# Performance work log

Measured on AMD Instinct MI355X. Metric: run time of the kernel, lower is better.

## Reference

```python
import jax, jax.numpy as jnp
import numpy as np

D_MODEL = 1024
N_HEADS = 16
HEAD_DIM = D_MODEL // N_HEADS


def setup_inputs() -> dict:
    key = jax.random.key(0)
    ks = jax.random.split(key, 5)
    B, T = 2, 2048
    x = jax.random.normal(ks[0], (B, T, D_MODEL), dtype=jnp.float32)
    s_in = 1.0 / np.sqrt(D_MODEL)
    W_qkv = jax.random.normal(ks[1], (D_MODEL, 3 * D_MODEL), dtype=jnp.float32) * s_in
    b_qkv = jnp.zeros((3 * D_MODEL,), dtype=jnp.float32)
    W_out = jax.random.normal(ks[2], (D_MODEL, D_MODEL), dtype=jnp.float32) * s_in
    b_out = jnp.zeros((D_MODEL,), dtype=jnp.float32)
    return {"x": x, "W_qkv": W_qkv, "b_qkv": b_qkv, "W_out": W_out, "b_out": b_out}


def reference(x, W_qkv, b_qkv, W_out, b_out):
    B, T, C = x.shape
    qkv = x @ W_qkv + b_qkv  # (B, T, 3C)
    q, k, v = jnp.split(qkv, 3, axis=-1)
    # (B, H, T, Dh)
    q = q.reshape(B, T, N_HEADS, HEAD_DIM).transpose(0, 2, 1, 3)
    k = k.reshape(B, T, N_HEADS, HEAD_DIM).transpose(0, 2, 1, 3)
    v = v.reshape(B, T, N_HEADS, HEAD_DIM).transpose(0, 2, 1, 3)
    scale = 1.0 / jnp.sqrt(jnp.asarray(HEAD_DIM, dtype=x.dtype))
    scores = jnp.einsum('bhqd,bhkd->bhqk', q, k) * scale  # (B, H, T, T)
    causal = jnp.tril(jnp.ones((T, T), dtype=bool))
    scores = jnp.where(causal[None, None], scores, jnp.asarray(-jnp.inf, dtype=scores.dtype))
    attn = jax.nn.softmax(scores, axis=-1)
    out = jnp.einsum('bhqk,bhkd->bhqd', attn, v)  # (B, H, T, Dh)
    out = out.transpose(0, 2, 1, 3).reshape(B, T, C)
    return out @ W_out + b_out
```

## Files before the change

kernel.cpp:

```cpp
#include <hip/hip_runtime.h>
#include <hip/hip_bf16.h>
#include <stdint.h>

typedef __bf16 bf16;
typedef __bf16 bf16x4 __attribute__((ext_vector_type(4)));
typedef __bf16 bf16x8 __attribute__((ext_vector_type(8)));
typedef float  f32x4  __attribute__((ext_vector_type(4)));

#define D_MODEL 1024
#define N_HEADS 16
#define HEAD_DIM 64
#define SEQ 2048
#define BATCH 2
#define LOG2E 1.4426950408889634f
#define NEG_SENT -3.0e4f
#define CAP 24.0f

__device__ __forceinline__ bf16x8 ld8(const bf16* p) { return *(const bf16x8*)p; }

__device__ __forceinline__ void async16(const bf16* g, bf16* l) {
  __builtin_amdgcn_global_load_lds(
      (const __attribute__((address_space(1))) void*)g,
      (__attribute__((address_space(3))) void*)l, 16, 0, 0);
}

__global__ __launch_bounds__(256)
void prep(const float* __restrict__ x, bf16* __restrict__ x16,
          const float* __restrict__ Wqkv, bf16* __restrict__ Wqkv_t,
          const float* __restrict__ Wout, bf16* __restrict__ Wout_t) {
  __shared__ float tile[32][33];
  const int blk = blockIdx.x, tid = threadIdx.x;
  if (blk < 4096) {
    int i = (blk * 256 + tid) * 4;
    float4 v = *(const float4*)&x[i];
    bf16 o[4] = {(bf16)v.x, (bf16)v.y, (bf16)v.z, (bf16)v.w};
    *(uint2*)&x16[i] = *(uint2*)o;
    return;
  }
  const float* in; bf16* out; int R, C, c0, r0;
  if (blk < 7168) {
    int b = blk - 4096;
    in = Wqkv; out = Wqkv_t; R = 1024; C = 3072;
    c0 = (b % 96) * 32; r0 = (b / 96) * 32;
  } else {
    int b = blk - 7168;
    in = Wout; out = Wout_t; R = 1024; C = 1024;
    c0 = (b % 32) * 32; r0 = (b / 32) * 32;
  }
  const int tx = tid & 31, ty = tid >> 5;
  #pragma unroll
  for (int i = 0; i < 32; i += 8)
    tile[ty + i][tx] = in[(size_t)(r0 + ty + i) * C + c0 + tx];
  __syncthreads();
  #pragma unroll
  for (int i = 0; i < 32; i += 8)
    out[(size_t)(c0 + ty + i) * R + r0 + tx] = (bf16)tile[tx][ty + i];
}

__global__ __launch_bounds__(256)
void gemm_bt(const bf16* __restrict__ A, const bf16* __restrict__ Bt,
             const float* __restrict__ bias, float* __restrict__ outf,
             bf16* __restrict__ Qp, bf16* __restrict__ Kp, bf16* __restrict__ Vtp,
             int N, int mode) {
  __shared__ __align__(16) bf16 shA[128 * 32];
  __shared__ __align__(16) bf16 shB[128 * 32];
  const int tid  = threadIdx.x;
  const int bm0  = blockIdx.y * 128, bn0 = blockIdx.x * 128;
  const int wave = tid >> 6, lane = tid & 63;
  const int quad = lane >> 4, l16 = lane & 15;
  const int wm = (wave >> 1) * 64, wn = (wave & 1) * 64;

  const int c_lo  = tid;
  const int row_lo = c_lo >> 2,  col_lo = (c_lo & 3) << 3;
  const int c_hi  = tid + 256;
  const int row_hi = c_hi >> 2,  col_hi = (c_hi & 3) << 3;
  const int cb_lo = (wave * 64) * 8;
  const int cb_hi = (256 + wave * 64) * 8;

  f32x4 acc[4][4];
  #pragma unroll
  for (int i = 0; i < 4; i++)
    #pragma unroll
    for (int j = 0; j < 4; j++)
      acc[i][j] = (f32x4){0.f, 0.f, 0.f, 0.f};

  for (int k0 = 0; k0 < 1024; k0 += 32) {
    async16(&A[(size_t)(bm0 + row_lo) * 1024 + k0 + col_lo], &shA[cb_lo]);
    async16(&A[(size_t)(bm0 + row_hi) * 1024 + k0 + col_hi], &shA[cb_hi]);
    async16(&Bt[(size_t)(bn0 + row_lo) * 1024 + k0 + col_lo], &shB[cb_lo]);
    async16(&Bt[(size_t)(bn0 + row_hi) * 1024 + k0 + col_hi], &shB[cb_hi]);
    __syncthreads();
    bf16x8 af[4], bg[4];
    #pragma unroll
    for (int i = 0; i < 4; i++)
      af[i] = ld8(&shA[(wm + i * 16 + l16) * 32 + quad * 8]);
    #pragma unroll
    for (int j = 0; j < 4; j++)
      bg[j] = ld8(&shB[(wn + j * 16 + l16) * 32 + quad * 8]);
    #pragma unroll
    for (int i = 0; i < 4; i++)
      #pragma unroll
      for (int j = 0; j < 4; j++)
        acc[i][j] = __builtin_amdgcn_mfma_f32_16x16x32_bf16(af[i], bg[j], acc[i][j], 0, 0, 0);
    __syncthreads();
  }

  #pragma unroll
  for (int i = 0; i < 4; i++) {
    #pragma unroll
    for (int j = 0; j < 4; j++) {
      int gn = bn0 + wn + j * 16 + l16;
      float bv = bias[gn];
      int gm0 = bm0 + wm + i * 16 + quad * 4;
      if (mode == 1) {
        #pragma unroll
        for (int r = 0; r < 4; r++)
          outf[(size_t)(gm0 + r) * N + gn] = acc[i][j][r] + bv;
      } else {
        int which = gn >> 10, rem = gn & 1023;
        int h = rem >> 6, d = rem & 63;
        int b = gm0 >> 11, t0 = gm0 & 2047;
        int bh = b * N_HEADS + h;
        if (which == 2) {
          bf16x4 vv = {(bf16)(acc[i][j][0] + bv), (bf16)(acc[i][j][1] + bv),
                       (bf16)(acc[i][j][2] + bv), (bf16)(acc[i][j][3] + bv)};
          *(bf16x4*)&Vtp[((size_t)bh * 64 + d) * SEQ + t0] = vv;
        } else {
          bf16* dst = (which == 0) ? Qp : Kp;
          #pragma unroll
          for (int r = 0; r < 4; r++)
            dst[((size_t)bh * SEQ + t0 + r) * 64 + d] = (bf16)(acc[i][j][r] + bv);
        }
      }
    }
  }
}

__global__ __launch_bounds__(256)
void gemm_out(const bf16* __restrict__ A, const bf16* __restrict__ Bt,
              const float* __restrict__ bias, float* __restrict__ outf) {
  __shared__ __align__(16) bf16 shA[64 * 32];
  __shared__ __align__(16) bf16 shB[128 * 32];
  const int tid  = threadIdx.x;
  const int bm0  = blockIdx.y * 64, bn0 = blockIdx.x * 128;
  const int wave = tid >> 6, lane = tid & 63;
  const int quad = lane >> 4, l16 = lane & 15;
  const int wn = wave * 32;

  f32x4 acc[4][2];
  #pragma unroll
  for (int i = 0; i < 4; i++)
    #pragma unroll
    for (int j = 0; j < 2; j++)
      acc[i][j] = (f32x4){0.f, 0.f, 0.f, 0.f};

  const int srow = tid >> 2, scol = (tid & 3) << 3;
  for (int k0 = 0; k0 < 1024; k0 += 32) {
    async16(&A[(size_t)(bm0 + srow) * 1024 + k0 + scol], &shA[tid * 8]);
    async16(&Bt[(size_t)(bn0 + srow) * 1024 + k0 + scol], &shB[tid * 8]);
    async16(&Bt[(size_t)(bn0 + 64 + srow) * 1024 + k0 + scol], &shB[(256 + tid) * 8]);
    __syncthreads();
    bf16x8 af[4], bg[2];
    #pragma unroll
    for (int i = 0; i < 4; i++)
      af[i] = ld8(&shA[(i * 16 + l16) * 32 + quad * 8]);
    #pragma unroll
    for (int j = 0; j < 2; j++)
      bg[j] = ld8(&shB[(wn + j * 16 + l16) * 32 + quad * 8]);
    #pragma unroll
    for (int i = 0; i < 4; i++)
      #pragma unroll
      for (int j = 0; j < 2; j++)
        acc[i][j] = __builtin_amdgcn_mfma_f32_16x16x32_bf16(af[i], bg[j], acc[i][j], 0, 0, 0);
    __syncthreads();
  }

  #pragma unroll
  for (int i = 0; i < 4; i++) {
    #pragma unroll
    for (int j = 0; j < 2; j++) {
      int gn = bn0 + wn + j * 16 + l16;
      float bv = bias[gn];
      int gm0 = bm0 + i * 16 + quad * 4;
      #pragma unroll
      for (int r = 0; r < 4; r++)
        outf[(size_t)(gm0 + r) * D_MODEL + gn] = acc[i][j][r] + bv;
    }
  }
}

__global__ __launch_bounds__(256)
void attn_k(const bf16* __restrict__ Qp, const bf16* __restrict__ Kp,
            const bf16* __restrict__ Vtp, bf16* __restrict__ Obuf) {
  __shared__ __align__(16) bf16 shK[2][64 * 64];
  __shared__ __align__(16) bf16 shV[2][64 * 64];
  __shared__ __align__(16) bf16 shPT[4][32 * 72];
  const int tid  = threadIdx.x;
  const int wave = tid >> 6, lane = tid & 63;
  const int quad = lane >> 4, l16 = lane & 15;
  const int bx = blockIdx.x;
  const int g = bx >> 5;
  const int qb = (g < 8) ? g : 23 - g;
  const int bh = bx & 31;
  const int qw0 = qb * 128 + wave * 32;

  const bf16* Qbh = Qp  + (size_t)bh * SEQ * 64;
  const bf16* Kbh = Kp  + (size_t)bh * SEQ * 64;
  const bf16* Vbh = Vtp + (size_t)bh * 64 * SEQ;

  const int kr_s = tid >> 3, kc_s = tid & 7;

  bf16x8 aQ[2][2];
  #pragma unroll
  for (int g2 = 0; g2 < 2; g2++)
    #pragma unroll
    for (int p = 0; p < 2; p++)
      aQ[g2][p] = ld8(&Qbh[(size_t)(qw0 + g2 * 16 + l16) * 64 + p * 32 + quad * 8]);

  f32x4 o0[4], o1[4];
  #pragma unroll
  for (int j = 0; j < 4; j++) { o0[j] = (f32x4){0.f,0.f,0.f,0.f}; o1[j] = (f32x4){0.f,0.f,0.f,0.f}; }
  f32x4 lacc0 = (f32x4){0.f,0.f,0.f,0.f}, lacc1 = (f32x4){0.f,0.f,0.f,0.f};
  const int qlane0 = qw0 + l16, qlane1 = qw0 + 16 + l16;
  const int xq = l16 & 7;

  const float SC = 0.125f * LOG2E;
  bf16* PT = shPT[wave];

  #pragma unroll
  for (int i = 0; i < 2; i++) {
    int kr = kr_s + i * 32;
    async16(&Kbh[(size_t)kr * 64 + (kc_s ^ (kr & 7)) * 8], &shK[0][(kr * 8 + kc_s) * 8]);
    async16(&Vbh[(size_t)kr * SEQ + (kc_s ^ (kr & 7)) * 8], &shV[0][(kr * 8 + kc_s) * 8]);
  }
  __syncthreads();

  const int NS = 2 * qb + 2;
  int cur = 0;
  for (int s = 0; s < NS; s++) {
    if (s + 1 < NS) {
      const int kb1 = (s + 1) * 64;
      #pragma unroll
      for (int i = 0; i < 2; i++) {
        int kr = kr_s + i * 32;
        async16(&Kbh[(size_t)(kb1 + kr) * 64 + (kc_s ^ (kr & 7)) * 8],
                &shK[cur ^ 1][(kr * 8 + kc_s) * 8]);
        async16(&Vbh[(size_t)kr * SEQ + kb1 + (kc_s ^ (kr & 7)) * 8],
                &shV[cur ^ 1][(kr * 8 + kc_s) * 8]);
      }
    }

    const int hb = s * 64;
    if (hb <= qw0 + 31) {
      const bf16* Kb = shK[cur];
      const bf16* Vb = shV[cur];

      f32x4 st0[4], st1[4];
      __builtin_amdgcn_s_setprio(1);
      #pragma unroll
      for (int c = 0; c < 4; c++) {
        int kr0 = c * 16 + l16;
        bf16x8 kf0 = ld8(&Kb[kr0 * 64 + ((quad    ) ^ xq) * 8]);
        bf16x8 kf1 = ld8(&Kb[kr0 * 64 + ((quad + 4) ^ xq) * 8]);
        f32x4 a0 = (f32x4){0.f,0.f,0.f,0.f};
        a0 = __builtin_amdgcn_mfma_f32_16x16x32_bf16(kf0, aQ[0][0], a0, 0, 0, 0);
        a0 = __builtin_amdgcn_mfma_f32_16x16x32_bf16(kf1, aQ[0][1], a0, 0, 0, 0);
        f32x4 a1 = (f32x4){0.f,0.f,0.f,0.f};
        a1 = __builtin_amdgcn_mfma_f32_16x16x32_bf16(kf0, aQ[1][0], a1, 0, 0, 0);
        a1 = __builtin_amdgcn_mfma_f32_16x16x32_bf16(kf1, aQ[1][1], a1, 0, 0, 0);
        st0[c] = a0; st1[c] = a1;
      }
      __builtin_amdgcn_s_setprio(0);

      if (hb + 63 > qw0) {
        #pragma unroll
        for (int c = 0; c < 4; c++)
          #pragma unroll
          for (int r = 0; r < 4; r++) {
            int key = hb + c * 16 + quad * 4 + r;
            if (key > qlane0) st0[c][r] = NEG_SENT;
            if (key > qlane1) st1[c][r] = NEG_SENT;
          }
      }

      #pragma unroll
      for (int c = 0; c < 4; c++) {
        #pragma unroll
        for (int r = 0; r < 4; r++) {
          st0[c][r] = exp2f(__builtin_fmaf(st0[c][r], SC, -CAP));
          st1[c][r] = exp2f(__builtin_fmaf(st1[c][r], SC, -CAP));
        }
        lacc0 += st0[c]; lacc1 += st1[c];
      }

      #pragma unroll
      for (int c = 0; c < 4; c++) {
        bf16x4 p0 = {(bf16)st0[c][0], (bf16)st0[c][1], (bf16)st0[c][2], (bf16)st0[c][3]};
        bf16x4 p1 = {(bf16)st1[c][0], (bf16)st1[c][1], (bf16)st1[c][2], (bf16)st1[c][3]};
        *(bf16x4*)&PT[l16 * 72 + c * 16 + quad * 4] = p0;
        *(bf16x4*)&PT[(16 + l16) * 72 + c * 16 + quad * 4] = p1;
      }
      asm volatile("s_waitcnt lgkmcnt(0)" ::: "memory");
      bf16x8 bP00 = ld8(&PT[l16 * 72 + quad * 8]);
      bf16x8 bP01 = ld8(&PT[l16 * 72 + 32 + quad * 8]);
      bf16x8 bP10 = ld8(&PT[(16 + l16) * 72 + quad * 8]);
      bf16x8 bP11 = ld8(&PT[(16 + l16) * 72 + 32 + quad * 8]);

      __builtin_amdgcn_s_setprio(1);
      #pragma unroll
      for (int j = 0; j < 4; j++) {
        int d = j * 16 + l16;
        bf16x8 v0 = ld8(&Vb[d * 64 + ((quad    ) ^ xq) * 8]);
        bf16x8 v1 = ld8(&Vb[d * 64 + ((quad + 4) ^ xq) * 8]);
        o0[j] = __builtin_amdgcn_mfma_f32_16x16x32_bf16(v0, bP00, o0[j], 0, 0, 0);
        o0[j] = __builtin_amdgcn_mfma_f32_16x16x32_bf16(v1, bP01, o0[j], 0, 0, 0);
        o1[j] = __builtin_amdgcn_mfma_f32_16x16x32_bf16(v0, bP10, o1[j], 0, 0, 0);
        o1[j] = __builtin_amdgcn_mfma_f32_16x16x32_bf16(v1, bP11, o1[j], 0, 0, 0);
      }
      __builtin_amdgcn_s_setprio(0);
    }

    __syncthreads();
    cur ^= 1;
  }

  const int b = bh >> 4, h = bh & 15;
  {
    float lr0 = (lacc0[0] + lacc0[1]) + (lacc0[2] + lacc0[3]);
    lr0 += __shfl_xor(lr0, 16, 64);
    lr0 += __shfl_xor(lr0, 32, 64);
    float lr1 = (lacc1[0] + lacc1[1]) + (lacc1[2] + lacc1[3]);
    lr1 += __shfl_xor(lr1, 16, 64);
    lr1 += __shfl_xor(lr1, 32, 64);
    float inv0 = 1.0f / lr0, inv1 = 1.0f / lr1;
    size_t base0 = ((size_t)(b * SEQ + qw0 + l16)) * D_MODEL + h * 64;
    size_t base1 = ((size_t)(b * SEQ + qw0 + 16 + l16)) * D_MODEL + h * 64;
    #pragma unroll
    for (int j = 0; j < 4; j++) {
      bf16x4 ov0 = {(bf16)(o0[j][0] * inv0), (bf16)(o0[j][1] * inv0),
                    (bf16)(o0[j][2] * inv0), (bf16)(o0[j][3] * inv0)};
      bf16x4 ov1 = {(bf16)(o1[j][0] * inv1), (bf16)(o1[j][1] * inv1),
                    (bf16)(o1[j][2] * inv1), (bf16)(o1[j][3] * inv1)};
      *(bf16x4*)&Obuf[base0 + j * 16 + quad * 4] = ov0;
      *(bf16x4*)&Obuf[base1 + j * 16 + quad * 4] = ov1;
    }
  }
}

extern "C" void kernel_launch(void* const* d_in, const int* in_sizes, int n_in,
                              void* d_out, int out_size, void* d_ws, size_t ws_size,
                              hipStream_t stream) {
  const float* x    = (const float*)d_in[0];
  const float* Wqkv = (const float*)d_in[1];
  const float* bqkv = (const float*)d_in[2];
  const float* Wout = (const float*)d_in[3];
  const float* bout = (const float*)d_in[4];
  float* out = (float*)d_out;

  char* ws = (char*)d_ws;
  bf16* x16    = (bf16*)(ws);
  bf16* Wqkv_t = (bf16*)(ws + 8388608);
  bf16* Wout_t = (bf16*)(ws + 14680064);
  bf16* Qp     = (bf16*)(ws + 16777216);
  bf16* Kp     = (bf16*)(ws + 25165824);
  bf16* Vtp    = (bf16*)(ws + 33554432);
  bf16* Obuf   = x16;

  prep<<<8192, 256, 0, stream>>>(x, x16, Wqkv, Wqkv_t, Wout, Wout_t);

  gemm_bt<<<dim3(3072 / 128, 4096 / 128), 256, 0, stream>>>(
      x16, Wqkv_t, bqkv, nullptr, Qp, Kp, Vtp, 3072, 0);

  attn_k<<<dim3(512), 256, 0, stream>>>(Qp, Kp, Vtp, Obuf);

  gemm_out<<<dim3(1024 / 128, 4096 / 64), 256, 0, stream>>>(
      Obuf, Wout_t, bout, out);
}
```

Baseline: 195.1 us.

## Use 512-thread attention blocks with 256-query tiles and halved P staging

The attention kernel now runs 8 waves per block, covering 256 queries instead of 128, so each K/V tile loaded into LDS is shared by twice as many waves. The grid becomes 8x32 with a simple query-block index, replacing the earlier balanced causal ordering. The per-wave P staging buffer is halved by writing the two 16-row halves one after the other, and V fragments are loaded before the P round trip. The risks are worse load balance across the causal triangle with fewer, larger blocks, fewer blocks overall (256 for 256 CUs), and extra LDS wait points.

```diff
diff --git a/kernel.cpp b/kernel.cpp
--- a/kernel.cpp
+++ b/kernel.cpp
@@ -189,20 +189,18 @@
   }
 }
 
-__global__ __launch_bounds__(256)
+__global__ __launch_bounds__(512)
 void attn_k(const bf16* __restrict__ Qp, const bf16* __restrict__ Kp,
             const bf16* __restrict__ Vtp, bf16* __restrict__ Obuf) {
   __shared__ __align__(16) bf16 shK[2][64 * 64];
   __shared__ __align__(16) bf16 shV[2][64 * 64];
-  __shared__ __align__(16) bf16 shPT[4][32 * 72];
+  __shared__ __align__(16) bf16 shPT[8][16 * 72];
   const int tid  = threadIdx.x;
   const int wave = tid >> 6, lane = tid & 63;
   const int quad = lane >> 4, l16 = lane & 15;
-  const int bx = blockIdx.x;
-  const int g = bx >> 5;
-  const int qb = (g < 8) ? g : 23 - g;
-  const int bh = bx & 31;
-  const int qw0 = qb * 128 + wave * 32;
+  const int qb = blockIdx.x;
+  const int bh = blockIdx.y;
+  const int qw0 = qb * 256 + wave * 32;
 
   const bf16* Qbh = Qp  + (size_t)bh * SEQ * 64;
   const bf16* Kbh = Kp  + (size_t)bh * SEQ * 64;
@@ -227,27 +225,19 @@
   const float SC = 0.125f * LOG2E;
   bf16* PT = shPT[wave];
 
-  #pragma unroll
-  for (int i = 0; i < 2; i++) {
-    int kr = kr_s + i * 32;
-    async16(&Kbh[(size_t)kr * 64 + (kc_s ^ (kr & 7)) * 8], &shK[0][(kr * 8 + kc_s) * 8]);
-    async16(&Vbh[(size_t)kr * SEQ + (kc_s ^ (kr & 7)) * 8], &shV[0][(kr * 8 + kc_s) * 8]);
-  }
+  async16(&Kbh[(size_t)kr_s * 64 + (kc_s ^ (kr_s & 7)) * 8], &shK[0][tid * 8]);
+  async16(&Vbh[(size_t)kr_s * SEQ + (kc_s ^ (kr_s & 7)) * 8], &shV[0][tid * 8]);
   __syncthreads();
 
-  const int NS = 2 * qb + 2;
+  const int NS = 4 * qb + 4;
   int cur = 0;
   for (int s = 0; s < NS; s++) {
     if (s + 1 < NS) {
       const int kb1 = (s + 1) * 64;
-      #pragma unroll
-      for (int i = 0; i < 2; i++) {
-        int kr = kr_s + i * 32;
-        async16(&Kbh[(size_t)(kb1 + kr) * 64 + (kc_s ^ (kr & 7)) * 8],
-                &shK[cur ^ 1][(kr * 8 + kc_s) * 8]);
-        async16(&Vbh[(size_t)kr * SEQ + kb1 + (kc_s ^ (kr & 7)) * 8],
-                &shV[cur ^ 1][(kr * 8 + kc_s) * 8]);
-      }
+      async16(&Kbh[(size_t)(kb1 + kr_s) * 64 + (kc_s ^ (kr_s & 7)) * 8],
+              &shK[cur ^ 1][tid * 8]);
+      async16(&Vbh[(size_t)kr_s * SEQ + kb1 + (kc_s ^ (kr_s & 7)) * 8],
+              &shV[cur ^ 1][tid * 8]);
     }
 
     const int hb = s * 64;
@@ -293,29 +283,39 @@
         lacc0 += st0[c]; lacc1 += st1[c];
       }
 
+      bf16x8 vf0[4], vf1[4];
+      #pragma unroll
+      for (int j = 0; j < 4; j++) {
+        int d = j * 16 + l16;
+        vf0[j] = ld8(&Vb[d * 64 + ((quad    ) ^ xq) * 8]);
+        vf1[j] = ld8(&Vb[d * 64 + ((quad + 4) ^ xq) * 8]);
+      }
+
       #pragma unroll
       for (int c = 0; c < 4; c++) {
         bf16x4 p0 = {(bf16)st0[c][0], (bf16)st0[c][1], (bf16)st0[c][2], (bf16)st0[c][3]};
-        bf16x4 p1 = {(bf16)st1[c][0], (bf16)st1[c][1], (bf16)st1[c][2], (bf16)st1[c][3]};
         *(bf16x4*)&PT[l16 * 72 + c * 16 + quad * 4] = p0;
-        *(bf16x4*)&PT[(16 + l16) * 72 + c * 16 + quad * 4] = p1;
       }
       asm volatile("s_waitcnt lgkmcnt(0)" ::: "memory");
       bf16x8 bP00 = ld8(&PT[l16 * 72 + quad * 8]);
       bf16x8 bP01 = ld8(&PT[l16 * 72 + 32 + quad * 8]);
-      bf16x8 bP10 = ld8(&PT[(16 + l16) * 72 + quad * 8]);
-      bf16x8 bP11 = ld8(&PT[(16 + l16) * 72 + 32 + quad * 8]);
+
+      #pragma unroll
+      for (int c = 0; c < 4; c++) {
+        bf16x4 p1 = {(bf16)st1[c][0], (bf16)st1[c][1], (bf16)st1[c][2], (bf16)st1[c][3]};
+        *(bf16x4*)&PT[l16 * 72 + c * 16 + quad * 4] = p1;
+      }
+      asm volatile("s_waitcnt lgkmcnt(0)" ::: "memory");
+      bf16x8 bP10 = ld8(&PT[l16 * 72 + quad * 8]);
+      bf16x8 bP11 = ld8(&PT[l16 * 72 + 32 + quad * 8]);
 
       __builtin_amdgcn_s_setprio(1);
       #pragma unroll
       for (int j = 0; j < 4; j++) {
-        int d = j * 16 + l16;
-        bf16x8 v0 = ld8(&Vb[d * 64 + ((quad    ) ^ xq) * 8]);
-        bf16x8 v1 = ld8(&Vb[d * 64 + ((quad + 4) ^ xq) * 8]);
-        o0[j] = __builtin_amdgcn_mfma_f32_16x16x32_bf16(v0, bP00, o0[j], 0, 0, 0);
-        o0[j] = __builtin_amdgcn_mfma_f32_16x16x32_bf16(v1, bP01, o0[j], 0, 0, 0);
-        o1[j] = __builtin_amdgcn_mfma_f32_16x16x32_bf16(v0, bP10, o1[j], 0, 0, 0);
-        o1[j] = __builtin_amdgcn_mfma_f32_16x16x32_bf16(v1, bP11, o1[j], 0, 0, 0);
+        o0[j] = __builtin_amdgcn_mfma_f32_16x16x32_bf16(vf0[j], bP00, o0[j], 0, 0, 0);
+        o0[j] = __builtin_amdgcn_mfma_f32_16x16x32_bf16(vf1[j], bP01, o0[j], 0, 0, 0);
+        o1[j] = __builtin_amdgcn_mfma_f32_16x16x32_bf16(vf0[j], bP10, o1[j], 0, 0, 0);
+        o1[j] = __builtin_amdgcn_mfma_f32_16x16x32_bf16(vf1[j], bP11, o1[j], 0, 0, 0);
       }
       __builtin_amdgcn_s_setprio(0);
     }
@@ -371,7 +371,7 @@
   gemm_bt<<<dim3(3072 / 128, 4096 / 128), 256, 0, stream>>>(
       x16, Wqkv_t, bqkv, nullptr, Qp, Kp, Vtp, 3072, 0);
 
-  attn_k<<<dim3(512), 256, 0, stream>>>(Qp, Kp, Vtp, Obuf);
+  attn_k<<<dim3(8, BATCH * N_HEADS), 512, 0, stream>>>(Qp, Kp, Vtp, Obuf);
 
   gemm_out<<<dim3(1024 / 128, 4096 / 64), 256, 0, stream>>>(
       Obuf, Wout_t, bout, out);
```

After: 209.7 us. 1.07x slower.

## Double key tile to 128 per barrier and shrink P transpose buffer

Applied to the files above, without the earlier changes.

The attention kernel now stages 128-key K and V tiles per double-buffered step and processes them as two 64-key halves. This halves the number of __syncthreads barriers and async-load rounds per block. The per-wave P staging buffer is shrunk to 16 rows, and the two query groups reuse it one after the other, which adds an extra LDS write/wait/read round per half. LDS use roughly doubles for K/V, which may lower occupancy.

```diff
diff --git a/kernel.cpp b/kernel.cpp
--- a/kernel.cpp
+++ b/kernel.cpp
@@ -192,9 +192,9 @@
 __global__ __launch_bounds__(256)
 void attn_k(const bf16* __restrict__ Qp, const bf16* __restrict__ Kp,
             const bf16* __restrict__ Vtp, bf16* __restrict__ Obuf) {
-  __shared__ __align__(16) bf16 shK[2][64 * 64];
-  __shared__ __align__(16) bf16 shV[2][64 * 64];
-  __shared__ __align__(16) bf16 shPT[4][32 * 72];
+  __shared__ __align__(16) bf16 shK[2][128 * 64];
+  __shared__ __align__(16) bf16 shV[2][64 * 128];
+  __shared__ __align__(16) bf16 shPT[4][16 * 72];
   const int tid  = threadIdx.x;
   const int wave = tid >> 6, lane = tid & 63;
   const int quad = lane >> 4, l16 = lane & 15;
@@ -208,8 +208,6 @@
   const bf16* Kbh = Kp  + (size_t)bh * SEQ * 64;
   const bf16* Vbh = Vtp + (size_t)bh * 64 * SEQ;
 
-  const int kr_s = tid >> 3, kc_s = tid & 7;
-
   bf16x8 aQ[2][2];
   #pragma unroll
   for (int g2 = 0; g2 < 2; g2++)
@@ -228,38 +226,54 @@
   bf16* PT = shPT[wave];
 
   #pragma unroll
-  for (int i = 0; i < 2; i++) {
-    int kr = kr_s + i * 32;
-    async16(&Kbh[(size_t)kr * 64 + (kc_s ^ (kr & 7)) * 8], &shK[0][(kr * 8 + kc_s) * 8]);
-    async16(&Vbh[(size_t)kr * SEQ + (kc_s ^ (kr & 7)) * 8], &shV[0][(kr * 8 + kc_s) * 8]);
+  for (int s2 = 0; s2 < 4; s2++) {
+    int id = tid + s2 * 256;
+    int kr = id >> 3, kc = id & 7;
+    async16(&Kbh[(size_t)kr * 64 + (kc ^ (kr & 7)) * 8], &shK[0][id * 8]);
+  }
+  #pragma unroll
+  for (int s2 = 0; s2 < 4; s2++) {
+    int id = tid + s2 * 256;
+    int vd = id >> 4, vc = id & 15;
+    int svc = (vc & 8) | ((vc & 7) ^ (vd & 7));
+    async16(&Vbh[(size_t)vd * SEQ + svc * 8], &shV[0][id * 8]);
   }
   __syncthreads();
 
-  const int NS = 2 * qb + 2;
+  const int NT = qb + 1;
   int cur = 0;
-  for (int s = 0; s < NS; s++) {
-    if (s + 1 < NS) {
-      const int kb1 = (s + 1) * 64;
-      #pragma unroll
-      for (int i = 0; i < 2; i++) {
-        int kr = kr_s + i * 32;
-        async16(&Kbh[(size_t)(kb1 + kr) * 64 + (kc_s ^ (kr & 7)) * 8],
-                &shK[cur ^ 1][(kr * 8 + kc_s) * 8]);
-        async16(&Vbh[(size_t)kr * SEQ + kb1 + (kc_s ^ (kr & 7)) * 8],
-                &shV[cur ^ 1][(kr * 8 + kc_s) * 8]);
-      }
-    }
-
-    const int hb = s * 64;
-    if (hb <= qw0 + 31) {
-      const bf16* Kb = shK[cur];
-      const bf16* Vb = shV[cur];
+  for (int kt = 0; kt < NT; kt++) {
+    if (kt + 1 < NT) {
+      const int kb1 = (kt + 1) * 128;
+      #pragma unroll
+      for (int s2 = 0; s2 < 4; s2++) {
+        int id = tid + s2 * 256;
+        int kr = id >> 3, kc = id & 7;
+        async16(&Kbh[(size_t)(kb1 + kr) * 64 + (kc ^ (kr & 7)) * 8],
+                &shK[cur ^ 1][id * 8]);
+      }
+      #pragma unroll
+      for (int s2 = 0; s2 < 4; s2++) {
+        int id = tid + s2 * 256;
+        int vd = id >> 4, vc = id & 15;
+        int svc = (vc & 8) | ((vc & 7) ^ (vd & 7));
+        async16(&Vbh[(size_t)vd * SEQ + kb1 + svc * 8], &shV[cur ^ 1][id * 8]);
+      }
+    }
+
+    const bf16* Kb = shK[cur];
+    const bf16* Vb = shV[cur];
+
+    #pragma unroll
+    for (int h = 0; h < 2; h++) {
+      const int hb = kt * 128 + h * 64;
+      if (hb > qw0 + 31) continue;
 
       f32x4 st0[4], st1[4];
       __builtin_amdgcn_s_setprio(1);
       #pragma unroll
       for (int c = 0; c < 4; c++) {
-        int kr0 = c * 16 + l16;
+        int kr0 = h * 64 + c * 16 + l16;
         bf16x8 kf0 = ld8(&Kb[kr0 * 64 + ((quad    ) ^ xq) * 8]);
         bf16x8 kf1 = ld8(&Kb[kr0 * 64 + ((quad + 4) ^ xq) * 8]);
         f32x4 a0 = (f32x4){0.f,0.f,0.f,0.f};
@@ -296,22 +310,27 @@
       #pragma unroll
       for (int c = 0; c < 4; c++) {
         bf16x4 p0 = {(bf16)st0[c][0], (bf16)st0[c][1], (bf16)st0[c][2], (bf16)st0[c][3]};
-        bf16x4 p1 = {(bf16)st1[c][0], (bf16)st1[c][1], (bf16)st1[c][2], (bf16)st1[c][3]};
         *(bf16x4*)&PT[l16 * 72 + c * 16 + quad * 4] = p0;
-        *(bf16x4*)&PT[(16 + l16) * 72 + c * 16 + quad * 4] = p1;
       }
       asm volatile("s_waitcnt lgkmcnt(0)" ::: "memory");
       bf16x8 bP00 = ld8(&PT[l16 * 72 + quad * 8]);
       bf16x8 bP01 = ld8(&PT[l16 * 72 + 32 + quad * 8]);
-      bf16x8 bP10 = ld8(&PT[(16 + l16) * 72 + quad * 8]);
-      bf16x8 bP11 = ld8(&PT[(16 + l16) * 72 + 32 + quad * 8]);
+
+      #pragma unroll
+      for (int c = 0; c < 4; c++) {
+        bf16x4 p1 = {(bf16)st1[c][0], (bf16)st1[c][1], (bf16)st1[c][2], (bf16)st1[c][3]};
+        *(bf16x4*)&PT[l16 * 72 + c * 16 + quad * 4] = p1;
+      }
+      asm volatile("s_waitcnt lgkmcnt(0)" ::: "memory");
+      bf16x8 bP10 = ld8(&PT[l16 * 72 + quad * 8]);
+      bf16x8 bP11 = ld8(&PT[l16 * 72 + 32 + quad * 8]);
 
       __builtin_amdgcn_s_setprio(1);
       #pragma unroll
       for (int j = 0; j < 4; j++) {
         int d = j * 16 + l16;
-        bf16x8 v0 = ld8(&Vb[d * 64 + ((quad    ) ^ xq) * 8]);
-        bf16x8 v1 = ld8(&Vb[d * 64 + ((quad + 4) ^ xq) * 8]);
+        bf16x8 v0 = ld8(&Vb[d * 128 + ((h * 8) | ((quad    ) ^ xq)) * 8]);
+        bf16x8 v1 = ld8(&Vb[d * 128 + ((h * 8) | ((quad + 4) ^ xq)) * 8]);
         o0[j] = __builtin_amdgcn_mfma_f32_16x16x32_bf16(v0, bP00, o0[j], 0, 0, 0);
         o0[j] = __builtin_amdgcn_mfma_f32_16x16x32_bf16(v1, bP01, o0[j], 0, 0, 0);
         o1[j] = __builtin_amdgcn_mfma_f32_16x16x32_bf16(v0, bP10, o1[j], 0, 0, 0);
```

After: 189.5 us. 2.9% less time.
